# Performance work log

Measured on AMD Instinct MI355X. Metric: run time of the kernel, lower is better.

## Reference

```python
import jax, jax.numpy as jnp
import numpy as np

T, B, E, H = 1024, 8, 1024, 16
DH = E // H
MASKED_BIAS = -10000.0


def setup_inputs() -> dict:
    key = jax.random.key(0)
    k1, k2, k3 = jax.random.split(key, 3)
    query = jax.random.normal(k1, (T, B, E), dtype=jnp.float32)
    # xavier-uniform-ish scale for the fused QKV and output projections
    qkv_w = jax.random.normal(k2, (3 * E, E), dtype=jnp.float32) * (1.0 / np.sqrt(2.0 * E))
    out_w = jax.random.normal(k3, (E, E), dtype=jnp.float32) * (1.0 / np.sqrt(E))
    return {
        "query": query,
        "qkv_w": qkv_w,
        "qkv_b": jnp.zeros((3 * E,), jnp.float32),
        "out_w": out_w,
        "out_b": jnp.zeros((E,), jnp.float32),
    }


def reference(query, qkv_w, qkv_b, out_w, out_b):
    # query: [T, B, E] (Time x Batch x Channel, fairseq convention)
    tgt_len, bsz, embed_dim = query.shape
    scaling = DH ** (-0.5)

    # Fused QKV projection (QuantLinear fake-quant treated as identity numerics)
    qkv = jnp.einsum("tbe,fe->tbf", query, qkv_w) + qkv_b  # [T, B, 3E]
    q, k, v = jnp.split(qkv, 3, axis=-1)
    q = q * scaling

    def to_heads(x):  # [T, B, E] -> [B*H, T, DH]
        return x.reshape(tgt_len, bsz * H, DH).transpose(1, 0, 2)

    q, k, v = to_heads(q), to_heads(k), to_heads(v)

    # attn_weights: [B*H, T, S]
    attn_weights = jnp.einsum("ntd,nsd->nts", q, k)

    # causal mask from the tril `bias` buffer with masked_bias fill
    causal = jnp.tril(jnp.ones((tgt_len, tgt_len), dtype=bool))
    attn_weights = jnp.where(causal[None, :, :], attn_weights,
                             jnp.asarray(MASKED_BIAS, attn_weights.dtype))

    attn_probs = jax.nn.softmax(attn_weights, axis=-1)
    # dropout p=0.0 in eval: no-op

    attn = jnp.einsum("nts,nsd->ntd", attn_probs, v)  # [B*H, T, DH]
    attn = attn.transpose(1, 0, 2).reshape(tgt_len, bsz, embed_dim)  # [T, B, E]

    out = jnp.einsum("tbe,fe->tbf", attn, out_w) + out_b
    return out
```

## Files before the change

### kernel.cpp

```cpp
#include <hip/hip_runtime.h>

typedef __attribute__((ext_vector_type(4))) float f32x4;
typedef __attribute__((ext_vector_type(16))) float f32x16;
typedef __attribute__((ext_vector_type(8))) short bf16x8;
typedef __attribute__((ext_vector_type(4))) unsigned short u16x4;
typedef __attribute__((ext_vector_type(4))) unsigned int u32x4;

#define T_DIM 1024
#define B_DIM 8
#define E_DIM 1024
#define H_DIM 16
#define DH 64

__device__ __forceinline__ unsigned short f2bf(float f) {
  unsigned int u = __builtin_bit_cast(unsigned int, f);
  u += 0x7fffu + ((u >> 16) & 1u);
  return (unsigned short)(u >> 16);
}

__device__ __forceinline__ unsigned int cvtpk_bf16(float lo, float hi) {
  unsigned int r;
  asm("v_cvt_pk_bf16_f32 %0, %1, %2" : "=v"(r) : "v"(lo), "v"(hi));
  return r;
}

__device__ __forceinline__ float exp2_hw(float x) {
  float r;
  asm("v_exp_f32 %0, %1" : "=v"(r) : "v"(x));
  return r;
}

__device__ __forceinline__ f32x4 mfma16(bf16x8 a, bf16x8 b, f32x4 c) {
  return __builtin_amdgcn_mfma_f32_16x16x32_bf16(a, b, c, 0, 0, 0);
}
__device__ __forceinline__ f32x16 mfma32(bf16x8 a, bf16x8 b, f32x16 c) {
  return __builtin_amdgcn_mfma_f32_32x32x16_bf16(a, b, c, 0, 0, 0);
}

__global__ __launch_bounds__(256) void cast_all(
    const float* __restrict__ q, const float* __restrict__ w1,
    const float* __restrict__ w2, unsigned short* __restrict__ dq,
    unsigned short* __restrict__ dw1, unsigned short* __restrict__ dw2) {
  int i = blockIdx.x * 256 + threadIdx.x;
  const float* src;
  unsigned short* dst;
  int off;
  if (i < 2097152)      { src = q;  dst = dq;  off = i; }
  else if (i < 2883584) { src = w1; dst = dw1; off = i - 2097152; }
  else                  { src = w2; dst = dw2; off = i - 2883584; }
  f32x4 v = *(const f32x4*)(src + (size_t)off * 4);
  u16x4 o;
  o[0] = f2bf(v[0]); o[1] = f2bf(v[1]); o[2] = f2bf(v[2]); o[3] = f2bf(v[3]);
  *(u16x4*)(dst + (size_t)off * 4) = o;
}

__device__ __forceinline__ void mainloop_128x128v2(
    const unsigned short* __restrict__ Ab,
    const unsigned short* __restrict__ Bb,
    unsigned short* smem, f32x4 acc[4][4]) {
  const int tid = threadIdx.x;
  const int wave = tid >> 6, lane = tid & 63;
  const int lr = lane & 15, lg = lane >> 4;
  const int x7 = lr & 7;
  const int wr = wave >> 1, wc = wave & 1;
  const int rlo = lane >> 3;
  const int csw = 8 * ((lane & 7) ^ rlo);

#define STG(KT, BUF)                                                            \
  {                                                                             \
    unsigned short* la_ = smem + (BUF) * 16384;                                 \
    unsigned short* lb_ = la_ + 8192;                                           \
    _Pragma("unroll")                                                           \
    for (int c_ = 0; c_ < 4; ++c_) {                                            \
      const int ins_ = wave * 4 + c_;                                           \
      __builtin_amdgcn_global_load_lds(                                         \
          (const __attribute__((address_space(1))) void*)(Ab + (size_t)(ins_ * 8 + rlo) * 1024 + (KT) * 64 + csw), \
          (__attribute__((address_space(3))) void*)(la_ + ins_ * 512), 16, 0, 0); \
      __builtin_amdgcn_global_load_lds(                                         \
          (const __attribute__((address_space(1))) void*)(Bb + (size_t)(ins_ * 8 + rlo) * 1024 + (KT) * 64 + csw), \
          (__attribute__((address_space(3))) void*)(lb_ + ins_ * 512), 16, 0, 0); \
    }                                                                           \
  }

#define COMPUTE(BUF)                                                            \
  {                                                                             \
    const unsigned short* la_ = smem + (BUF) * 16384;                           \
    const unsigned short* ha_ = la_ + (wr * 64) * 64;                           \
    const unsigned short* hb_ = la_ + 8192 + (wc * 64) * 64;                    \
    _Pragma("unroll")                                                           \
    for (int ks_ = 0; ks_ < 2; ++ks_) {                                         \
      bf16x8 af_[4], bf_[4];                                                    \
      const int cu_ = (((ks_ * 4 + lg) ^ x7) << 3);                             \
      _Pragma("unroll")                                                         \
      for (int i_ = 0; i_ < 4; ++i_) {                                          \
        af_[i_] = *(const bf16x8*)(ha_ + (i_ * 16 + lr) * 64 + cu_);            \
        bf_[i_] = *(const bf16x8*)(hb_ + (i_ * 16 + lr) * 64 + cu_);            \
      }                                                                         \
      __builtin_amdgcn_s_setprio(1);                                            \
      _Pragma("unroll")                                                         \
      for (int mi_ = 0; mi_ < 4; ++mi_)                                         \
        _Pragma("unroll")                                                       \
        for (int ni_ = 0; ni_ < 4; ++ni_)                                       \
          acc[mi_][ni_] = mfma16(af_[mi_], bf_[ni_], acc[mi_][ni_]);            \
      __builtin_amdgcn_s_setprio(0);                                            \
    }                                                                           \
  }

  STG(0, 0)
  asm volatile("s_waitcnt vmcnt(0)" ::: "memory");
  __builtin_amdgcn_s_barrier();
  __builtin_amdgcn_sched_barrier(0);

#pragma unroll 2
  for (int t = 0; t < 16; ++t) {
    if (t < 15) {
      STG(t + 1, (t + 1) & 1)
      asm volatile("s_waitcnt vmcnt(8)" ::: "memory");
    } else {
      asm volatile("s_waitcnt vmcnt(0)" ::: "memory");
    }
    __builtin_amdgcn_s_barrier();
    __builtin_amdgcn_sched_barrier(0);
    COMPUTE(t & 1)
    __builtin_amdgcn_s_barrier();
    __builtin_amdgcn_sched_barrier(0);
  }
#undef STG
#undef COMPUTE
}

__global__ __launch_bounds__(256) void gemm_qkv13(
    const unsigned short* __restrict__ A, const unsigned short* __restrict__ W,
    const float* __restrict__ bias,
    unsigned short* __restrict__ Qh, unsigned short* __restrict__ Kh,
    unsigned short* __restrict__ Vh) {
  __shared__ unsigned short smem[32768];
  const int bid = blockIdx.x;
  const int xcd = bid & 7, i = bid >> 3;
  const int m0 = (xcd * 8 + (i & 7)) * 128;
  const int n0 = (i >> 3) * 128;

  f32x4 acc[4][4];
  const f32x4 z4 = {0.f, 0.f, 0.f, 0.f};
#pragma unroll
  for (int a = 0; a < 4; ++a)
#pragma unroll
    for (int b2 = 0; b2 < 4; ++b2) acc[a][b2] = z4;

  mainloop_128x128v2(A + (size_t)m0 * 1024, W + (size_t)n0 * 1024, smem, acc);

  const int lane = threadIdx.x & 63, wave = threadIdx.x >> 6;
  const int lr = lane & 15, lg = lane >> 4;
  const int wr = wave >> 1, wc = wave & 1;
#pragma unroll
  for (int mf = 0; mf < 4; ++mf)
#pragma unroll
    for (int nf = 0; nf < 4; ++nf)
#pragma unroll
      for (int j = 0; j < 4; ++j) {
        int m = m0 + wr * 64 + mf * 16 + lg * 4 + j;
        int f = n0 + wc * 64 + nf * 16 + lr;
        float v = acc[mf][nf][j] + bias[f];
        int t = m >> 3, b = m & 7;
        int e = f & 1023, h = e >> 6, d = e & 63;
        int which = f >> 10;
        size_t idx = ((size_t)(b * 16 + h) * T_DIM + t) * DH + d;
        if (which == 0)      Qh[idx] = f2bf(v * 0.18033688011111772f);
        else if (which == 1) Kh[idx] = f2bf(v);
        else                 Vh[idx] = f2bf(v);
      }
}

__global__ __launch_bounds__(256) void gemm_out13(
    const unsigned short* __restrict__ A, const unsigned short* __restrict__ W,
    const float* __restrict__ bias, float* __restrict__ out) {
  __shared__ unsigned short smem[32768];
  const int bid = blockIdx.x;
  const int xcd = bid & 7, i = bid >> 3;
  const int m0 = (xcd * 8 + (i & 7)) * 128;
  const int n0 = (i >> 3) * 128;

  f32x4 acc[4][4];
  const f32x4 z4 = {0.f, 0.f, 0.f, 0.f};
#pragma unroll
  for (int a = 0; a < 4; ++a)
#pragma unroll
    for (int b2 = 0; b2 < 4; ++b2) acc[a][b2] = z4;

  mainloop_128x128v2(A + (size_t)m0 * 1024, W + (size_t)n0 * 1024, smem, acc);

  const int lane = threadIdx.x & 63, wave = threadIdx.x >> 6;
  const int lr = lane & 15, lg = lane >> 4;
  const int wr = wave >> 1, wc = wave & 1;
#pragma unroll
  for (int mf = 0; mf < 4; ++mf)
#pragma unroll
    for (int nf = 0; nf < 4; ++nf)
#pragma unroll
      for (int j = 0; j < 4; ++j) {
        int m = m0 + wr * 64 + mf * 16 + lg * 4 + j;
        int f = n0 + wc * 64 + nf * 16 + lr;
        out[(size_t)m * E_DIM + f] = acc[mf][nf][j] + bias[f];
      }
}

__global__ __launch_bounds__(256) void transpose_v(
    const unsigned short* __restrict__ Vh, unsigned short* __restrict__ Vt) {
  __shared__ unsigned short tile[64][72];
  const int n = blockIdx.x, t0 = blockIdx.y * 64;
  const int tid = threadIdx.x;
  const int r = tid >> 3, c8 = tid & 7;
#pragma unroll
  for (int it = 0; it < 2; ++it) {
    int row = it * 32 + r;
    bf16x8 v = *(const bf16x8*)(Vh + ((size_t)n * T_DIM + t0 + row) * DH + c8 * 8);
    *(bf16x8*)&tile[row][c8 * 8] = v;
  }
  __syncthreads();
#pragma unroll
  for (int it = 0; it < 2; ++it) {
    int d = it * 32 + r;
    bf16x8 ov;
#pragma unroll
    for (int jj = 0; jj < 8; ++jj) ov[jj] = (short)tile[c8 * 8 + jj][d];
    *(bf16x8*)(Vt + ((size_t)n * DH + d) * T_DIM + t0 + c8 * 8) = ov;
  }
}

__global__ __launch_bounds__(256) void flash_attn6(
    const unsigned short* __restrict__ Qh, const unsigned short* __restrict__ Kh,
    const unsigned short* __restrict__ Vt, unsigned short* __restrict__ attn) {
  __shared__ unsigned short lds[2][2][4096];
  const int tid = threadIdx.x;
  const int wave = tid >> 6, lane = tid & 63;
  const int lq = lane & 31, hi = lane >> 5;
  const int bid = blockIdx.x;
  const int qt = 7 - (bid >> 7);
  const int n = bid & 127;
  const int b = n >> 4, h = n & 15;
  const int q0w = qt * 128 + wave * 32;
  const int q = q0w + lq;
  const int nbb = 2 * qt + 2;
  const int mynb = (q0w + 95) >> 6;

  const unsigned short* kh_n = Kh + (size_t)n * (T_DIM * DH);
  const unsigned short* vt_n = Vt + (size_t)n * (DH * T_DIM);

  const int rlo = lane >> 3;
  const int csw = 8 * ((lane & 7) ^ rlo);

#define STAGE(S0, BUF)                                                          \
  {                                                                             \
    _Pragma("unroll")                                                           \
    for (int m_ = 0; m_ < 2; ++m_) {                                            \
      const int instr_ = wave * 2 + m_;                                         \
      const int r_ = instr_ * 8 + rlo;                                          \
      __builtin_amdgcn_global_load_lds(                                         \
          (const __attribute__((address_space(1))) void*)(kh_n + (size_t)((S0) + r_) * DH + csw), \
          (__attribute__((address_space(3))) void*)(&lds[BUF][0][instr_ * 512]), 16, 0, 0); \
      __builtin_amdgcn_global_load_lds(                                         \
          (const __attribute__((address_space(1))) void*)(vt_n + (size_t)r_ * T_DIM + (S0) + csw), \
          (__attribute__((address_space(3))) void*)(&lds[BUF][1][instr_ * 512]), 16, 0, 0); \
    }                                                                           \
  }

  bf16x8 qf[4];
  const unsigned short* qp = Qh + ((size_t)n * T_DIM + q) * DH + hi * 8;
#pragma unroll
  for (int kk = 0; kk < 4; ++kk) qf[kk] = *(const bf16x8*)(qp + kk * 16);

  f32x16 o0, o1;
#pragma unroll
  for (int r = 0; r < 16; ++r) { o0[r] = 0.f; o1[r] = 0.f; }
  float m_run = -1e30f, l_run = 0.f;

  STAGE(0, 0);
  asm volatile("s_waitcnt vmcnt(0)");
  __builtin_amdgcn_s_barrier();

  const int swzr = (lq & 7) << 4;

  for (int i = 0; i < nbb; ++i) {
    const int cur = i & 1;
    if (i + 1 < nbb) {
      STAGE((i + 1) * 64, cur ^ 1);
      asm volatile("s_waitcnt vmcnt(4)");
    } else {
      asm volatile("s_waitcnt vmcnt(0)");
    }
    __builtin_amdgcn_s_barrier();
    __builtin_amdgcn_sched_barrier(0);

    if (i < mynb) {
      const int s0 = i * 64;
      const unsigned short* kb = lds[cur][0];
      const unsigned short* vb = lds[cur][1];
      f32x16 sA, sB;
#pragma unroll
      for (int r = 0; r < 16; ++r) { sA[r] = 0.f; sB[r] = 0.f; }
      __builtin_amdgcn_s_setprio(1);
#pragma unroll
      for (int kk = 0; kk < 4; ++kk) {
        const int cb = ((kk * 32 + hi * 16) ^ swzr) >> 1;
        bf16x8 ka = *(const bf16x8*)(kb + lq * 64 + cb);
        bf16x8 kbf = *(const bf16x8*)(kb + (32 + lq) * 64 + cb);
        sA = mfma32(ka, qf[kk], sA);
        sB = mfma32(kbf, qf[kk], sB);
      }
      __builtin_amdgcn_s_setprio(0);
      if (i == mynb - 1) {
#pragma unroll
        for (int r = 0; r < 16; ++r) {
          int sp = s0 + (r & 3) + 8 * (r >> 2) + 4 * hi;
          if (sp > q)      sA[r] = -10000.0f;
          if (sp + 32 > q) sB[r] = -10000.0f;
        }
      }
      float t0 = fmaxf(sA[0], sB[0]), t1 = fmaxf(sA[1], sB[1]);
      float t2 = fmaxf(sA[2], sB[2]), t3 = fmaxf(sA[3], sB[3]);
#pragma unroll
      for (int r = 4; r < 16; r += 4) {
        t0 = fmaxf(t0, fmaxf(sA[r], sB[r]));
        t1 = fmaxf(t1, fmaxf(sA[r + 1], sB[r + 1]));
        t2 = fmaxf(t2, fmaxf(sA[r + 2], sB[r + 2]));
        t3 = fmaxf(t3, fmaxf(sA[r + 3], sB[r + 3]));
      }
      float tmax = fmaxf(fmaxf(t0, t1), fmaxf(t2, t3));
      tmax = fmaxf(tmax, __shfl_xor(tmax, 32));
      if (__any(tmax - m_run > 11.5f)) {
        float m_new = fmaxf(m_run, tmax);
        float sc = exp2_hw(m_run - m_new);
        l_run *= sc;
#pragma unroll
        for (int r = 0; r < 16; ++r) { o0[r] *= sc; o1[r] *= sc; }
        m_run = m_new;
      }
      float r0 = 0.f, r1 = 0.f, r2 = 0.f, r3 = 0.f;
#pragma unroll
      for (int r = 0; r < 16; r += 4) {
        sA[r] = exp2_hw(sA[r] - m_run);         r0 += sA[r];
        sA[r + 1] = exp2_hw(sA[r + 1] - m_run); r1 += sA[r + 1];
        sA[r + 2] = exp2_hw(sA[r + 2] - m_run); r2 += sA[r + 2];
        sA[r + 3] = exp2_hw(sA[r + 3] - m_run); r3 += sA[r + 3];
      }
#pragma unroll
      for (int r = 0; r < 16; r += 4) {
        sB[r] = exp2_hw(sB[r] - m_run);         r0 += sB[r];
        sB[r + 1] = exp2_hw(sB[r + 1] - m_run); r1 += sB[r + 1];
        sB[r + 2] = exp2_hw(sB[r + 2] - m_run); r2 += sB[r + 2];
        sB[r + 3] = exp2_hw(sB[r + 3] - m_run); r3 += sB[r + 3];
      }
      float rs = (r0 + r1) + (r2 + r3);
      rs += __shfl_xor(rs, 32);
      l_run += rs;
      unsigned int pk[16];
#pragma unroll
      for (int ii = 0; ii < 8; ++ii) pk[ii]     = cvtpk_bf16(sA[2 * ii], sA[2 * ii + 1]);
#pragma unroll
      for (int ii = 0; ii < 8; ++ii) pk[8 + ii] = cvtpk_bf16(sB[2 * ii], sB[2 * ii + 1]);
      __builtin_amdgcn_s_setprio(1);
#pragma unroll
      for (int ks = 0; ks < 4; ++ks) {
        unsigned int A0 = pk[ks * 4 + 0], A1 = pk[ks * 4 + 1];
        unsigned int B0 = pk[ks * 4 + 2], B1 = pk[ks * 4 + 3];
        unsigned int xA0 = __shfl_xor(A0, 32), xA1 = __shfl_xor(A1, 32);
        unsigned int xB0 = __shfl_xor(B0, 32), xB1 = __shfl_xor(B1, 32);
        u32x4 uu;
        uu[0] = hi ? xB0 : A0;
        uu[1] = hi ? xB1 : A1;
        uu[2] = hi ? B0 : xA0;
        uu[3] = hi ? B1 : xA1;
        bf16x8 pf = __builtin_bit_cast(bf16x8, uu);
        const int cb = ((ks * 32 + hi * 16) ^ swzr) >> 1;
        bf16x8 v0 = *(const bf16x8*)(vb + lq * 64 + cb);
        bf16x8 v1 = *(const bf16x8*)(vb + (32 + lq) * 64 + cb);
        o0 = mfma32(v0, pf, o0);
        o1 = mfma32(v1, pf, o1);
      }
      __builtin_amdgcn_s_setprio(0);
    }
    __builtin_amdgcn_s_barrier();
  }
#undef STAGE

  const float inv = 1.0f / l_run;
  unsigned short* op = attn + ((size_t)q * B_DIM + b) * E_DIM + h * DH;
#pragma unroll
  for (int g = 0; g < 4; ++g) {
    u16x4 w0, w1;
#pragma unroll
    for (int jj = 0; jj < 4; ++jj) {
      w0[jj] = f2bf(o0[g * 4 + jj] * inv);
      w1[jj] = f2bf(o1[g * 4 + jj] * inv);
    }
    int d = 8 * g + 4 * hi;
    *(u16x4*)(op + d) = w0;
    *(u16x4*)(op + 32 + d) = w1;
  }
}

extern "C" void kernel_launch(void* const* d_in, const int* in_sizes, int n_in,
                              void* d_out, int out_size, void* d_ws, size_t ws_size,
                              hipStream_t stream) {
  const float* query = (const float*)d_in[0];
  const float* qkv_w = (const float*)d_in[1];
  const float* qkv_b = (const float*)d_in[2];
  const float* out_w = (const float*)d_in[3];
  const float* out_b = (const float*)d_in[4];
  float* out = (float*)d_out;

  char* ws = (char*)d_ws;
  unsigned short* Abf  = (unsigned short*)(ws);
  unsigned short* Wbf  = (unsigned short*)(ws + (size_t)(16u << 20));
  unsigned short* OWbf = (unsigned short*)(ws + (size_t)(22u << 20));
  unsigned short* Qh   = (unsigned short*)(ws + (size_t)(24u << 20));
  unsigned short* Kh   = (unsigned short*)(ws + (size_t)(40u << 20));
  unsigned short* Vh   = (unsigned short*)(ws + (size_t)(56u << 20));
  unsigned short* Vt   = (unsigned short*)(ws + (size_t)(72u << 20));
  unsigned short* attn = Abf;

  cast_all<<<12288, 256, 0, stream>>>(query, qkv_w, out_w, Abf, Wbf, OWbf);
  gemm_qkv13<<<1536, 256, 0, stream>>>(Abf, Wbf, qkv_b, Qh, Kh, Vh);
  transpose_v<<<dim3(128, 16), 256, 0, stream>>>(Vh, Vt);
  flash_attn6<<<1024, 256, 0, stream>>>(Qh, Kh, Vt, attn);
  gemm_out13<<<512, 256, 0, stream>>>(attn, OWbf, out_b, out);
}
```

Measured before the change: 155.6 us.

## Widen QKV GEMM to 128x256 tiles with triple buffering and fused V transpose

The QKV projection GEMM now uses 512-thread blocks computing 128x256 output tiles, with a three-stage LDS ring buffer (147 KB dynamic shared memory) for deeper prefetch. The epilogue writes V directly in transposed layout, removing the separate transpose_v kernel launch and its extra round trip through memory. Risks: the large LDS footprint limits occupancy to one block per CU. The transposed V stores are strided in t, so writes may be less coalesced.

Result: slower. 169.2 us (+8.7%).

```diff
diff --git a/kernel.cpp b/kernel.cpp
--- a/kernel.cpp
+++ b/kernel.cpp
@@ -54,7 +54,7 @@
   *(u16x4*)(dst + (size_t)off * 4) = o;
 }
 
-__device__ __forceinline__ void mainloop_128x128v2(
+__device__ __forceinline__ void mainloop_128x256(
     const unsigned short* __restrict__ Ab,
     const unsigned short* __restrict__ Bb,
     unsigned short* smem, f32x4 acc[4][4]) {
@@ -62,21 +62,25 @@
   const int wave = tid >> 6, lane = tid & 63;
   const int lr = lane & 15, lg = lane >> 4;
   const int x7 = lr & 7;
-  const int wr = wave >> 1, wc = wave & 1;
+  const int wr = wave >> 2, wc = wave & 3;
   const int rlo = lane >> 3;
   const int csw = 8 * ((lane & 7) ^ rlo);
 
 #define STG(KT, BUF)                                                            \
   {                                                                             \
-    unsigned short* la_ = smem + (BUF) * 16384;                                 \
+    unsigned short* la_ = smem + (BUF) * 24576;                                 \
     unsigned short* lb_ = la_ + 8192;                                           \
+    _Pragma("unroll")                                                           \
+    for (int c_ = 0; c_ < 2; ++c_) {                                            \
+      const int ins_ = wave * 2 + c_;                                           \
+      __builtin_amdgcn_global_load_lds(                                         \
+          (const __attribute__((address_space(1))) void*)(Ab + (size_t)(ins_ * 8 + rlo) * 1024 + (KT) * 64 + csw), \
+          (__attribute__((address_space(3))) void*)(la_ + ins_ * 512), 16, 0, 0); \
+    }                                                                           \
     _Pragma("unroll")                                                           \
     for (int c_ = 0; c_ < 4; ++c_) {                                            \
       const int ins_ = wave * 4 + c_;                                           \
       __builtin_amdgcn_global_load_lds(                                         \
-          (const __attribute__((address_space(1))) void*)(Ab + (size_t)(ins_ * 8 + rlo) * 1024 + (KT) * 64 + csw), \
-          (__attribute__((address_space(3))) void*)(la_ + ins_ * 512), 16, 0, 0); \
-      __builtin_amdgcn_global_load_lds(                                         \
           (const __attribute__((address_space(1))) void*)(Bb + (size_t)(ins_ * 8 + rlo) * 1024 + (KT) * 64 + csw), \
           (__attribute__((address_space(3))) void*)(lb_ + ins_ * 512), 16, 0, 0); \
     }                                                                           \
@@ -84,7 +88,7 @@
 
 #define COMPUTE(BUF)                                                            \
   {                                                                             \
-    const unsigned short* la_ = smem + (BUF) * 16384;                           \
+    const unsigned short* la_ = smem + (BUF) * 24576;                           \
     const unsigned short* ha_ = la_ + (wr * 64) * 64;                           \
     const unsigned short* hb_ = la_ + 8192 + (wc * 64) * 64;                    \
     _Pragma("unroll")                                                           \
@@ -106,6 +110,80 @@
     }                                                                           \
   }
 
+#define ENDT(WAITSTR)                                                           \
+  asm volatile("s_waitcnt " WAITSTR ::: "memory");                              \
+  __builtin_amdgcn_s_barrier();                                                 \
+  __builtin_amdgcn_sched_barrier(0);
+
+  STG(0, 0) STG(1, 1)
+  ENDT("vmcnt(6)")
+
+  for (int tt = 0; tt < 12; tt += 3) {
+    STG(tt + 2, 2) COMPUTE(0) ENDT("vmcnt(6)")
+    STG(tt + 3, 0) COMPUTE(1) ENDT("vmcnt(6)")
+    STG(tt + 4, 1) COMPUTE(2) ENDT("vmcnt(6)")
+  }
+  STG(14, 2) COMPUTE(0) ENDT("vmcnt(6)")
+  STG(15, 0) COMPUTE(1) ENDT("vmcnt(6)")
+  COMPUTE(2) ENDT("vmcnt(0)")
+  COMPUTE(0)
+#undef STG
+#undef COMPUTE
+#undef ENDT
+}
+
+__device__ __forceinline__ void mainloop_128x128v2(
+    const unsigned short* __restrict__ Ab,
+    const unsigned short* __restrict__ Bb,
+    unsigned short* smem, f32x4 acc[4][4]) {
+  const int tid = threadIdx.x;
+  const int wave = tid >> 6, lane = tid & 63;
+  const int lr = lane & 15, lg = lane >> 4;
+  const int x7 = lr & 7;
+  const int wr = wave >> 1, wc = wave & 1;
+  const int rlo = lane >> 3;
+  const int csw = 8 * ((lane & 7) ^ rlo);
+
+#define STG(KT, BUF)                                                            \
+  {                                                                             \
+    unsigned short* la_ = smem + (BUF) * 16384;                                 \
+    unsigned short* lb_ = la_ + 8192;                                           \
+    _Pragma("unroll")                                                           \
+    for (int c_ = 0; c_ < 4; ++c_) {                                            \
+      const int ins_ = wave * 4 + c_;                                           \
+      __builtin_amdgcn_global_load_lds(                                         \
+          (const __attribute__((address_space(1))) void*)(Ab + (size_t)(ins_ * 8 + rlo) * 1024 + (KT) * 64 + csw), \
+          (__attribute__((address_space(3))) void*)(la_ + ins_ * 512), 16, 0, 0); \
+      __builtin_amdgcn_global_load_lds(                                         \
+          (const __attribute__((address_space(1))) void*)(Bb + (size_t)(ins_ * 8 + rlo) * 1024 + (KT) * 64 + csw), \
+          (__attribute__((address_space(3))) void*)(lb_ + ins_ * 512), 16, 0, 0); \
+    }                                                                           \
+  }
+
+#define COMPUTE(BUF)                                                            \
+  {                                                                             \
+    const unsigned short* la_ = smem + (BUF) * 16384;                           \
+    const unsigned short* ha_ = la_ + (wr * 64) * 64;                           \
+    const unsigned short* hb_ = la_ + 8192 + (wc * 64) * 64;                    \
+    _Pragma("unroll")                                                           \
+    for (int ks_ = 0; ks_ < 2; ++ks_) {                                         \
+      bf16x8 af_[4], bf_[4];                                                    \
+      const int cu_ = (((ks_ * 4 + lg) ^ x7) << 3);                             \
+      _Pragma("unroll")                                                         \
+      for (int i_ = 0; i_ < 4; ++i_) {                                          \
+        af_[i_] = *(const bf16x8*)(ha_ + (i_ * 16 + lr) * 64 + cu_);            \
+        bf_[i_] = *(const bf16x8*)(hb_ + (i_ * 16 + lr) * 64 + cu_);            \
+      }                                                                         \
+      __builtin_amdgcn_s_setprio(1);                                            \
+      _Pragma("unroll")                                                         \
+      for (int mi_ = 0; mi_ < 4; ++mi_)                                         \
+        _Pragma("unroll")                                                       \
+        for (int ni_ = 0; ni_ < 4; ++ni_)                                       \
+          acc[mi_][ni_] = mfma16(af_[mi_], bf_[ni_], acc[mi_][ni_]);            \
+      __builtin_amdgcn_s_setprio(0);                                            \
+    }                                                                           \
+  }
+
   STG(0, 0)
   asm volatile("s_waitcnt vmcnt(0)" ::: "memory");
   __builtin_amdgcn_s_barrier();
@@ -129,16 +207,16 @@
 #undef COMPUTE
 }
 
-__global__ __launch_bounds__(256) void gemm_qkv13(
+__global__ __launch_bounds__(512) void gemm_qkv14(
     const unsigned short* __restrict__ A, const unsigned short* __restrict__ W,
     const float* __restrict__ bias,
     unsigned short* __restrict__ Qh, unsigned short* __restrict__ Kh,
-    unsigned short* __restrict__ Vh) {
-  __shared__ unsigned short smem[32768];
+    unsigned short* __restrict__ Vt) {
+  extern __shared__ unsigned short smem[];
   const int bid = blockIdx.x;
   const int xcd = bid & 7, i = bid >> 3;
   const int m0 = (xcd * 8 + (i & 7)) * 128;
-  const int n0 = (i >> 3) * 128;
+  const int n0 = (i >> 3) * 256;
 
   f32x4 acc[4][4];
   const f32x4 z4 = {0.f, 0.f, 0.f, 0.f};
@@ -147,11 +225,11 @@
 #pragma unroll
     for (int b2 = 0; b2 < 4; ++b2) acc[a][b2] = z4;
 
-  mainloop_128x128v2(A + (size_t)m0 * 1024, W + (size_t)n0 * 1024, smem, acc);
+  mainloop_128x256(A + (size_t)m0 * 1024, W + (size_t)n0 * 1024, smem, acc);
 
   const int lane = threadIdx.x & 63, wave = threadIdx.x >> 6;
   const int lr = lane & 15, lg = lane >> 4;
-  const int wr = wave >> 1, wc = wave & 1;
+  const int wr = wave >> 2, wc = wave & 3;
 #pragma unroll
   for (int mf = 0; mf < 4; ++mf)
 #pragma unroll
@@ -164,10 +242,12 @@
         int t = m >> 3, b = m & 7;
         int e = f & 1023, h = e >> 6, d = e & 63;
         int which = f >> 10;
-        size_t idx = ((size_t)(b * 16 + h) * T_DIM + t) * DH + d;
-        if (which == 0)      Qh[idx] = f2bf(v * 0.18033688011111772f);
-        else if (which == 1) Kh[idx] = f2bf(v);
-        else                 Vh[idx] = f2bf(v);
+        if (which == 0)
+          Qh[((size_t)(b * 16 + h) * T_DIM + t) * DH + d] = f2bf(v * 0.18033688011111772f);
+        else if (which == 1)
+          Kh[((size_t)(b * 16 + h) * T_DIM + t) * DH + d] = f2bf(v);
+        else
+          Vt[((size_t)(b * 16 + h) * DH + d) * T_DIM + t] = f2bf(v);
       }
 }
 
@@ -202,29 +282,6 @@
         int f = n0 + wc * 64 + nf * 16 + lr;
         out[(size_t)m * E_DIM + f] = acc[mf][nf][j] + bias[f];
       }
-}
-
-__global__ __launch_bounds__(256) void transpose_v(
-    const unsigned short* __restrict__ Vh, unsigned short* __restrict__ Vt) {
-  __shared__ unsigned short tile[64][72];
-  const int n = blockIdx.x, t0 = blockIdx.y * 64;
-  const int tid = threadIdx.x;
-  const int r = tid >> 3, c8 = tid & 7;
-#pragma unroll
-  for (int it = 0; it < 2; ++it) {
-    int row = it * 32 + r;
-    bf16x8 v = *(const bf16x8*)(Vh + ((size_t)n * T_DIM + t0 + row) * DH + c8 * 8);
-    *(bf16x8*)&tile[row][c8 * 8] = v;
-  }
-  __syncthreads();
-#pragma unroll
-  for (int it = 0; it < 2; ++it) {
-    int d = it * 32 + r;
-    bf16x8 ov;
-#pragma unroll
-    for (int jj = 0; jj < 8; ++jj) ov[jj] = (short)tile[c8 * 8 + jj][d];
-    *(bf16x8*)(Vt + ((size_t)n * DH + d) * T_DIM + t0 + c8 * 8) = ov;
-  }
 }
 
 __global__ __launch_bounds__(256) void flash_attn6(
@@ -415,13 +472,11 @@
   unsigned short* OWbf = (unsigned short*)(ws + (size_t)(22u << 20));
   unsigned short* Qh   = (unsigned short*)(ws + (size_t)(24u << 20));
   unsigned short* Kh   = (unsigned short*)(ws + (size_t)(40u << 20));
-  unsigned short* Vh   = (unsigned short*)(ws + (size_t)(56u << 20));
   unsigned short* Vt   = (unsigned short*)(ws + (size_t)(72u << 20));
   unsigned short* attn = Abf;
 
   cast_all<<<12288, 256, 0, stream>>>(query, qkv_w, out_w, Abf, Wbf, OWbf);
-  gemm_qkv13<<<1536, 256, 0, stream>>>(Abf, Wbf, qkv_b, Qh, Kh, Vh);
-  transpose_v<<<dim3(128, 16), 256, 0, stream>>>(Vh, Vt);
+  gemm_qkv14<<<768, 512, 147456, stream>>>(Abf, Wbf, qkv_b, Qh, Kh, Vt);
   flash_attn6<<<1024, 256, 0, stream>>>(Qh, Kh, Vt, attn);
   gemm_out13<<<512, 256, 0, stream>>>(attn, OWbf, out_b, out);
 }
```
